# Kernel tuning notes

Measured on AMD Instinct MI355X. Metric: run time of the kernel, lower is better.

## Reference

```python
import jax, jax.numpy as jnp
import numpy as np

B, T, D, HS = 4, 4096, 512, 64


def setup_inputs() -> dict:
    key = jax.random.key(0)
    kx, kd, kk, kq, kv = jax.random.split(key, 5)
    X = jax.random.normal(kx, (B, T, D), dtype=jnp.float32)
    dag = jax.random.randint(kd, (T, T), 0, 2, dtype=jnp.int32)
    scale = 1.0 / np.sqrt(D).astype(np.float32)
    Wk = jax.random.normal(kk, (D, HS), dtype=jnp.float32) * scale
    Wq = jax.random.normal(kq, (D, HS), dtype=jnp.float32) * scale
    Wv = jax.random.normal(kv, (D, HS), dtype=jnp.float32) * scale
    return {"X": X, "dag": dag, "Wk": Wk, "Wq": Wq, "Wv": Wv}


def reference(X, dag, Wk, Wq, Wv):
    # Projections (nn.Linear without bias): [B,T,HS]
    K = X @ Wk
    Q = X @ Wq
    V = X @ Wv
    hs = Q.shape[-1]
    # Dense scores [B,T,T]
    QK = jnp.einsum('bid,bjd->bij', Q, K) / np.float32(np.sqrt(hs))
    mask = (dag == 0)  # [T,T], True -> -inf
    # Rows fully masked would softmax to NaN in torch; the module zeroes them.
    row_dead = jnp.all(mask, axis=-1)  # [T]
    neg_inf = jnp.asarray(-jnp.inf, QK.dtype)
    scores = jnp.where(mask, neg_inf, QK)
    # Neutralize dead rows before softmax to avoid NaN, then zero them out
    scores = jnp.where(row_dead[:, None], jnp.zeros((), QK.dtype), scores)
    att = jax.nn.softmax(scores, axis=-1)
    att = jnp.where(row_dead[:, None], jnp.zeros((), att.dtype), att)
    # Transposed AV matmul: out[b,j,h] = sum_i att[b,i,j] * V[b,i,h]
    out = jnp.einsum('bij,bih->bjh', att, V)
    # Swish activation
    return out * jax.nn.sigmoid(out)
```

## Files before the change

kernel.cpp:

```cpp
#include <hip/hip_runtime.h>
#include <hip/hip_bf16.h>
#include <math.h>

#define BB 4
#define TT 4096
#define DD 512
#define HH 64
#define TW 128

typedef unsigned int u32;
typedef unsigned short u16;
typedef float f32x16 __attribute__((ext_vector_type(16)));
typedef __bf16 bf16x8 __attribute__((ext_vector_type(8)));

#define SC 0.18033688011112042f

static __device__ __forceinline__ u16 f2b(float f) {
    __hip_bfloat16 h = __float2bfloat16(f);
    return __builtin_bit_cast(u16, h);
}
static __device__ __forceinline__ float b2f(u16 x) {
    return __builtin_bit_cast(float, (u32)x << 16);
}
static __device__ __forceinline__ u32 pk2(float a, float b) {
    return (u32)f2b(a) | ((u32)f2b(b) << 16);
}
static __device__ __forceinline__ bf16x8 ldf(const u16* p) {
    uint4 u = *(const uint4*)p;
    return __builtin_bit_cast(bf16x8, u);
}
static __device__ __forceinline__ bf16x8 c8(uint4 u) {
    return __builtin_bit_cast(bf16x8, u);
}
static __device__ __forceinline__ void swap32(u32& a, u32& b) {
    asm("v_permlane32_swap_b32 %0, %1" : "+v"(a), "+v"(b));
}


__global__ __launch_bounds__(256) void pack_kernel(const int* __restrict__ dag,
                                                   u32* __restrict__ bits2,
                                                   u32* __restrict__ bitsTT,
                                                   const float* __restrict__ Wq,
                                                   const float* __restrict__ Wk,
                                                   const float* __restrict__ Wv,
                                                   u16* __restrict__ Wt) {
    if (blockIdx.x >= 2048) {
        const int wb = blockIdx.x - 2048;
        const int m = wb >> 3, sub = wb & 7;
        const float* W = (m == 0) ? Wq : (m == 1) ? Wk : Wv;
        const int t = threadIdx.x;
        const int n = sub * 8 + (t >> 5);
        const int k0 = (t & 31) * 16;
        u16 buf[16];
#pragma unroll
        for (int k = 0; k < 16; ++k) buf[k] = f2b(W[(size_t)(k0 + k) * HH + n]);
        uint4* dst = (uint4*)(Wt + ((size_t)m * 64 + n) * DD + k0);
        dst[0] = *(uint4*)buf;
        dst[1] = *(uint4*)(buf + 8);
        return;
    }
    const int unit = blockIdx.x * 4 + (threadIdx.x >> 6);
    const int lane = threadIdx.x & 63;
    const int i64 = unit >> 7;
    const int j32 = unit & 127;
    const int i = i64 * 64 + lane;
    const int* p = dag + (size_t)i * TT + j32 * 32;
    u32 rw = 0;
#pragma unroll
    for (int c = 0; c < 32; c += 4) {
        int4 v = *(const int4*)(p + c);
        rw |= (v.x != 0 ? 1u : 0u) << c;
        rw |= (v.y != 0 ? 1u : 0u) << (c + 1);
        rw |= (v.z != 0 ? 1u : 0u) << (c + 2);
        rw |= (v.w != 0 ? 1u : 0u) << (c + 3);
    }
    bits2[(size_t)j32 * TT + i] = rw;
    u32 myw = 0;
#pragma unroll
    for (int c = 0; c < 32; ++c) {
        unsigned long long m = __ballot((rw >> c) & 1);
        u32 part = (lane < 32) ? (u32)m : (u32)(m >> 32);
        if ((lane & 31) == c) myw = part;
    }
    bitsTT[(size_t)(i64 * 2 + (lane >> 5)) * TT + j32 * 32 + (lane & 31)] = myw;
}

__global__ __launch_bounds__(384) void proj_kernel(const float* __restrict__ X,
                                                   const u16* __restrict__ Wt,
                                                   u16* __restrict__ QF,
                                                   u16* __restrict__ KF,
                                                   u16* __restrict__ VF) {
    const int w = threadIdx.x >> 6, lane = threadIdx.x & 63;
    const int m = w % 3, rg = w / 3;
    const int l31 = lane & 31, hf = lane >> 5;
    const int tile = blockIdx.x * 2 + rg;
    const int row0 = tile * 32;
    const float* xr = X + (size_t)(row0 + l31) * DD + hf * 8;
    const u16* wbase = Wt + (size_t)m * 64 * DD + hf * 8;

    f32x16 acc[2] = {};

    for (int kt = 0; kt < 32; ++kt) {
        float4 x0 = *(const float4*)(xr + kt * 16);
        float4 x1 = *(const float4*)(xr + kt * 16 + 4);
        uint4 aw;
        aw.x = pk2(x0.x, x0.y);
        aw.y = pk2(x0.z, x0.w);
        aw.z = pk2(x1.x, x1.y);
        aw.w = pk2(x1.z, x1.w);
        bf16x8 xa = __builtin_bit_cast(bf16x8, aw);
        const u16* wk = wbase + kt * 16;
#pragma unroll
        for (int nt = 0; nt < 2; ++nt) {
            bf16x8 wb = ldf(wk + (size_t)(nt * 32 + l31) * DD);
            acc[nt] = __builtin_amdgcn_mfma_f32_32x32x16_bf16(xa, wb, acc[nt], 0, 0, 0);
        }
    }
    const float sc = (m == 0) ? SC : 1.0f;
    if (m < 2) {
        u16* dst = (m == 0) ? QF : KF;
        const int kth = l31 >> 4, hfp = (l31 >> 3) & 1, e = l31 & 7;
#pragma unroll
        for (int nt = 0; nt < 2; ++nt)
#pragma unroll
            for (int r = 0; r < 16; ++r) {
                int rl = (r & 3) + 8 * (r >> 2) + 4 * hf;
                dst[(size_t)tile * 2048 + (nt * 2 + kth) * 512 + (rl + hfp * 32) * 8 + e]
                    = f2b(acc[nt][r] * sc);
            }
    } else {
#pragma unroll
        for (int nt = 0; nt < 2; ++nt)
#pragma unroll
            for (int r = 0; r < 16; ++r) {
                int rl = (r & 3) + 8 * (r >> 2) + 4 * hf;
                VF[(size_t)tile * 2048 + (nt * 2 + (rl >> 4)) * 512
                   + (l31 + ((rl >> 3) & 1) * 32) * 8 + (rl & 7)] = f2b(acc[nt][r]);
            }
    }
}

__global__ __launch_bounds__(512, 2) void stats_kernel(const u16* __restrict__ QF,
                                                       const u16* __restrict__ KF,
                                                       const u32* __restrict__ bits2,
                                                       float* __restrict__ cOut) {
    __shared__ float Lsh[8][128];
    const int bid = blockIdx.x;
    const int b = (bid & 7) >> 1;
    const int u = (bid & 1) * 32 + (bid >> 3);
    const int itg0 = u * 2;
    const int i0 = itg0 * 32;
    const int w = threadIdx.x >> 6, lane = threadIdx.x & 63;
    const int l31 = lane & 31, hf = lane >> 5;

    bf16x8 qfA[4], qfB[4];
    const u16* qbase = QF + (size_t)(b * 128 + itg0) * 2048 + lane * 8;
#pragma unroll
    for (int kt = 0; kt < 4; ++kt) {
        qfA[kt] = ldf(qbase + kt * 512);
        qfB[kt] = ldf(qbase + 2048 + kt * 512);
    }

    const u16* kf0 = KF + (size_t)b * 128 * 2048 + lane * 8;

    float LpA = 0.f, LpB = 0.f;
    for (int t = 0; t < 16; ++t) {
        const int jt = w + t * 8;
        const u16* kb = kf0 + (size_t)jt * 2048;
        u32 mwA = bits2[(size_t)jt * TT + i0 + l31];
        u32 mwB = bits2[(size_t)jt * TT + i0 + 32 + l31];

        bf16x8 k0 = ldf(kb), k1 = ldf(kb + 512), k2 = ldf(kb + 1024), k3 = ldf(kb + 1536);
        __builtin_amdgcn_s_setprio(1);
        f32x16 sA = {}, sB = {};
        sA = __builtin_amdgcn_mfma_f32_32x32x16_bf16(k0, qfA[0], sA, 0, 0, 0);
        sB = __builtin_amdgcn_mfma_f32_32x32x16_bf16(k0, qfB[0], sB, 0, 0, 0);
        sA = __builtin_amdgcn_mfma_f32_32x32x16_bf16(k1, qfA[1], sA, 0, 0, 0);
        sB = __builtin_amdgcn_mfma_f32_32x32x16_bf16(k1, qfB[1], sB, 0, 0, 0);
        sA = __builtin_amdgcn_mfma_f32_32x32x16_bf16(k2, qfA[2], sA, 0, 0, 0);
        sB = __builtin_amdgcn_mfma_f32_32x32x16_bf16(k2, qfB[2], sB, 0, 0, 0);
        sA = __builtin_amdgcn_mfma_f32_32x32x16_bf16(k3, qfA[3], sA, 0, 0, 0);
        sB = __builtin_amdgcn_mfma_f32_32x32x16_bf16(k3, qfB[3], sB, 0, 0, 0);
        __builtin_amdgcn_s_setprio(0);
        u32 mrA = __builtin_amdgcn_alignbit(mwA, mwA, hf * 4);
        u32 mrB = __builtin_amdgcn_alignbit(mwB, mwB, hf * 4);
#pragma unroll
        for (int r = 0; r < 16; ++r) {
            const int pos = (r & 3) + 8 * (r >> 2);
            float eA = __builtin_amdgcn_exp2f(sA[r]);
            float eB = __builtin_amdgcn_exp2f(sB[r]);
            LpA += ((mrA >> pos) & 1) ? eA : 0.f;
            LpB += ((mrB >> pos) & 1) ? eB : 0.f;
        }
    }
    Lsh[w][lane] = LpA;
    Lsh[w][64 + lane] = LpB;
    __syncthreads();
    if (threadIdx.x < 64) {
        const int g = threadIdx.x >> 5, il = threadIdx.x & 31;
        float L = 0.f;
#pragma unroll
        for (int q = 0; q < 8; ++q) L += Lsh[q][g * 64 + il] + Lsh[q][g * 64 + il + 32];
        cOut[(size_t)b * TT + i0 + g * 32 + il] = (L > 0.f) ? 1.f / L : 0.f;
    }
}

__global__ __launch_bounds__(256) void scalev_kernel(const u16* __restrict__ VF,
                                                     const float* __restrict__ cB,
                                                     u16* __restrict__ VF2) {
    const int bid = blockIdx.x;
    const int b = (bid & 7) >> 1;
    const int itg = (bid & 1) * 64 + (bid >> 3);
    const int tile = b * 128 + itg;
    const int q = threadIdx.x >> 6, ln = threadIdx.x & 63;
    const float* c = cB + (size_t)b * TT + itg * 32 + (q & 1) * 16 + (ln >> 5) * 8;
    float4 c0 = *(const float4*)c;
    float4 c1 = *(const float4*)(c + 4);
    const u16* p = VF + (size_t)tile * 2048 + q * 512 + ln * 8;
    uint4 v = *(const uint4*)p;
    u16* ve = (u16*)&v;
    ve[0] = f2b(b2f(ve[0]) * c0.x);
    ve[1] = f2b(b2f(ve[1]) * c0.y);
    ve[2] = f2b(b2f(ve[2]) * c0.z);
    ve[3] = f2b(b2f(ve[3]) * c0.w);
    ve[4] = f2b(b2f(ve[4]) * c1.x);
    ve[5] = f2b(b2f(ve[5]) * c1.y);
    ve[6] = f2b(b2f(ve[6]) * c1.z);
    ve[7] = f2b(b2f(ve[7]) * c1.w);
    *(uint4*)(VF2 + (size_t)tile * 2048 + q * 512 + ln * 8) = v;
}

__global__ __launch_bounds__(512, 2) void out_kernel(const u16* __restrict__ QF,
                                                     const u16* __restrict__ KF,
                                                     const u16* __restrict__ VF2,
                                                     const u32* __restrict__ bitsTT,
                                                     float* __restrict__ out) {
    __shared__ float red[2][4][2048];
    const int bid = blockIdx.x;
    const int b = (bid & 7) >> 1;
    const int u = (bid & 1) * 32 + (bid >> 3);
    const int jt0 = u * 2;
    const int j0 = jt0 * 32;
    const int w = threadIdx.x >> 6, lane = threadIdx.x & 63;
    const int l31 = lane & 31, hf = lane >> 5;

    bf16x8 kfA[4], kfB[4];
    const u16* kbase = KF + (size_t)(b * 128 + jt0) * 2048 + lane * 8;
#pragma unroll
    for (int kt = 0; kt < 4; ++kt) {
        kfA[kt] = ldf(kbase + kt * 512);
        kfB[kt] = ldf(kbase + 2048 + kt * 512);
    }

    const u16* qf0 = QF + (size_t)b * 128 * 2048 + lane * 8;
    const u16* vf0 = VF2 + (size_t)b * 128 * 2048 + lane * 8;

    f32x16 accA0 = {}, accA1 = {}, accB0 = {}, accB1 = {};

    for (int t = 0; t < 16; ++t) {
        const int it = w + t * 8;
        const u16* qb = qf0 + (size_t)it * 2048;
        const u16* vb = vf0 + (size_t)it * 2048;
        u32 mwA = bitsTT[(size_t)it * TT + j0 + l31];
        u32 mwB = bitsTT[(size_t)it * TT + j0 + 32 + l31];

        bf16x8 q0 = ldf(qb), q1 = ldf(qb + 512), q2 = ldf(qb + 1024), q3 = ldf(qb + 1536);
        __builtin_amdgcn_s_setprio(1);
        f32x16 sA = {}, sB = {};
        sA = __builtin_amdgcn_mfma_f32_32x32x16_bf16(q0, kfA[0], sA, 0, 0, 0);
        sB = __builtin_amdgcn_mfma_f32_32x32x16_bf16(q0, kfB[0], sB, 0, 0, 0);
        sA = __builtin_amdgcn_mfma_f32_32x32x16_bf16(q1, kfA[1], sA, 0, 0, 0);
        sB = __builtin_amdgcn_mfma_f32_32x32x16_bf16(q1, kfB[1], sB, 0, 0, 0);
        sA = __builtin_amdgcn_mfma_f32_32x32x16_bf16(q2, kfA[2], sA, 0, 0, 0);
        sB = __builtin_amdgcn_mfma_f32_32x32x16_bf16(q2, kfB[2], sB, 0, 0, 0);
        sA = __builtin_amdgcn_mfma_f32_32x32x16_bf16(q3, kfA[3], sA, 0, 0, 0);
        sB = __builtin_amdgcn_mfma_f32_32x32x16_bf16(q3, kfB[3], sB, 0, 0, 0);
        __builtin_amdgcn_s_setprio(0);

        u32 mrA = __builtin_amdgcn_alignbit(mwA, mwA, hf * 4);
        u32 mrB = __builtin_amdgcn_alignbit(mwB, mwB, hf * 4);

        float pA[16], pB[16];
#pragma unroll
        for (int r = 0; r < 16; ++r) {
            const int pos = (r & 3) + 8 * (r >> 2);
            float eA = __builtin_amdgcn_exp2f(sA[r]);
            float eB = __builtin_amdgcn_exp2f(sB[r]);
            pA[r] = ((mrA >> pos) & 1) ? eA : 0.f;
            pB[r] = ((mrB >> pos) & 1) ? eB : 0.f;
        }

        bf16x8 v00 = ldf(vb), v01 = ldf(vb + 512), v10 = ldf(vb + 1024), v11 = ldf(vb + 1536);

#pragma unroll
        for (int k2 = 0; k2 < 2; ++k2) {
            u32 aA  = pk2(pA[8 * k2 + 0], pA[8 * k2 + 1]);
            u32 bA  = pk2(pA[8 * k2 + 2], pA[8 * k2 + 3]);
            u32 cA  = pk2(pA[8 * k2 + 4], pA[8 * k2 + 5]);
            u32 dA  = pk2(pA[8 * k2 + 6], pA[8 * k2 + 7]);
            swap32(aA, cA);
            swap32(bA, dA);
            uint4 awA = {aA, bA, cA, dA};
            bf16x8 paA = __builtin_bit_cast(bf16x8, awA);
            u32 aB  = pk2(pB[8 * k2 + 0], pB[8 * k2 + 1]);
            u32 bB  = pk2(pB[8 * k2 + 2], pB[8 * k2 + 3]);
            u32 cB2 = pk2(pB[8 * k2 + 4], pB[8 * k2 + 5]);
            u32 dB  = pk2(pB[8 * k2 + 6], pB[8 * k2 + 7]);
            swap32(aB, cB2);
            swap32(bB, dB);
            uint4 awB = {aB, bB, cB2, dB};
            bf16x8 paB = __builtin_bit_cast(bf16x8, awB);
            bf16x8 v0 = (k2 == 0) ? v00 : v01;
            bf16x8 v1 = (k2 == 0) ? v10 : v11;
            __builtin_amdgcn_s_setprio(1);
            accA0 = __builtin_amdgcn_mfma_f32_32x32x16_bf16(paA, v0, accA0, 0, 0, 0);
            accB0 = __builtin_amdgcn_mfma_f32_32x32x16_bf16(paB, v0, accB0, 0, 0, 0);
            accA1 = __builtin_amdgcn_mfma_f32_32x32x16_bf16(paA, v1, accA1, 0, 0, 0);
            accB1 = __builtin_amdgcn_mfma_f32_32x32x16_bf16(paB, v1, accB1, 0, 0, 0);
            __builtin_amdgcn_s_setprio(0);
        }
    }

    if (w >= 4) {
#pragma unroll
        for (int r = 0; r < 16; ++r) {
            int jl = (r & 3) + 8 * (r >> 2) + 4 * hf;
            red[0][w - 4][jl * 64 + l31] = accA0[r];
            red[0][w - 4][jl * 64 + 32 + l31] = accA1[r];
            red[1][w - 4][jl * 64 + l31] = accB0[r];
            red[1][w - 4][jl * 64 + 32 + l31] = accB1[r];
        }
    }
    __syncthreads();
    if (w < 4) {
#pragma unroll
        for (int r = 0; r < 16; ++r) {
            int jl = (r & 3) + 8 * (r >> 2) + 4 * hf;
            red[0][w][jl * 64 + l31] += accA0[r];
            red[0][w][jl * 64 + 32 + l31] += accA1[r];
            red[1][w][jl * 64 + l31] += accB0[r];
            red[1][w][jl * 64 + 32 + l31] += accB1[r];
        }
    }
    __syncthreads();
    {
        const int idx = threadIdx.x * 8;
        const int g3 = idx >> 11, e = idx & 2047;
        float vv[8];
#pragma unroll
        for (int q = 0; q < 8; ++q) {
            int ee = e + q;
            float v = red[g3][0][ee] + red[g3][1][ee] + red[g3][2][ee] + red[g3][3][ee];
            vv[q] = v / (1.f + __expf(-v));
        }
        const int jl = e >> 6, hc = e & 63;
        float* dst = out + ((size_t)b * TT + (jt0 + g3) * 32 + jl) * HH + hc;
        *(float4*)dst = make_float4(vv[0], vv[1], vv[2], vv[3]);
        *(float4*)(dst + 4) = make_float4(vv[4], vv[5], vv[6], vv[7]);
    }
}

extern "C" void kernel_launch(void* const* d_in, const int* in_sizes, int n_in,
                              void* d_out, int out_size, void* d_ws, size_t ws_size,
                              hipStream_t stream) {
    const float* X  = (const float*)d_in[0];
    const int*  dag = (const int*)d_in[1];
    const float* Wk = (const float*)d_in[2];
    const float* Wq = (const float*)d_in[3];
    const float* Wv = (const float*)d_in[4];
    float* out = (float*)d_out;

    char* ws = (char*)d_ws;
    u16*   QF    = (u16*)ws;
    u16*   KF    = (u16*)(ws + (2u << 20));
    u16*   VF    = (u16*)(ws + (4u << 20));
    u16*   VF2   = (u16*)(ws + (6u << 20));
    u32*   bits2 = (u32*)(ws + (8u << 20));
    u32*   bitsTT= (u32*)(ws + (10u << 20));
    u16*   Wt    = (u16*)(ws + (12u << 20));
    float* cB    = (float*)(ws + (12u << 20) + (256u << 10));

    pack_kernel<<<2048 + 24, 256, 0, stream>>>(dag, bits2, bitsTT, Wq, Wk, Wv, Wt);
    proj_kernel<<<256, 384, 0, stream>>>(X, Wt, QF, KF, VF);
    stats_kernel<<<256, 512, 0, stream>>>(QF, KF, bits2, cB);
    scalev_kernel<<<512, 256, 0, stream>>>(VF, cB, VF2);
    out_kernel<<<256, 512, 0, stream>>>(QF, KF, VF2, bitsTT, out);
}
```

Baseline: 94.52 us.

## Fuse V scaling into stats kernel and co-schedule dag packing with projection

The separate V-scaling kernel is folded into the end of the stats kernel: each block keeps its row normalisers in shared memory and scales its own two V tiles, so the cB round trip through global memory and one launch go away. The dag bit-packing moves into the projection kernel as extra blocks, so packing and projection run in one launch and can overlap. Weight transposition becomes its own small kernel that runs ahead. The extra packing blocks are launched with 384 threads and 128 of them exit at once, which wastes some slots. The stats kernel also gains a tail phase with an extra barrier.

```diff
diff --git a/kernel.cpp b/kernel.cpp
--- a/kernel.cpp
+++ b/kernel.cpp
@@ -29,67 +29,65 @@
     uint4 u = *(const uint4*)p;
     return __builtin_bit_cast(bf16x8, u);
 }
-static __device__ __forceinline__ bf16x8 c8(uint4 u) {
-    return __builtin_bit_cast(bf16x8, u);
-}
 static __device__ __forceinline__ void swap32(u32& a, u32& b) {
     asm("v_permlane32_swap_b32 %0, %1" : "+v"(a), "+v"(b));
 }
 
 
-__global__ __launch_bounds__(256) void pack_kernel(const int* __restrict__ dag,
-                                                   u32* __restrict__ bits2,
-                                                   u32* __restrict__ bitsTT,
-                                                   const float* __restrict__ Wq,
-                                                   const float* __restrict__ Wk,
-                                                   const float* __restrict__ Wv,
-                                                   u16* __restrict__ Wt) {
-    if (blockIdx.x >= 2048) {
-        const int wb = blockIdx.x - 2048;
-        const int m = wb >> 3, sub = wb & 7;
-        const float* W = (m == 0) ? Wq : (m == 1) ? Wk : Wv;
-        const int t = threadIdx.x;
-        const int n = sub * 8 + (t >> 5);
-        const int k0 = (t & 31) * 16;
-        u16 buf[16];
-#pragma unroll
-        for (int k = 0; k < 16; ++k) buf[k] = f2b(W[(size_t)(k0 + k) * HH + n]);
-        uint4* dst = (uint4*)(Wt + ((size_t)m * 64 + n) * DD + k0);
-        dst[0] = *(uint4*)buf;
-        dst[1] = *(uint4*)(buf + 8);
+__global__ __launch_bounds__(256) void wtr_kernel(const float* __restrict__ Wq,
+                                                  const float* __restrict__ Wk,
+                                                  const float* __restrict__ Wv,
+                                                  u16* __restrict__ Wt) {
+    const int wb = blockIdx.x;
+    const int m = wb >> 3, sub = wb & 7;
+    const float* W = (m == 0) ? Wq : (m == 1) ? Wk : Wv;
+    const int t = threadIdx.x;
+    const int n = sub * 8 + (t >> 5);
+    const int k0 = (t & 31) * 16;
+    u16 buf[16];
+#pragma unroll
+    for (int k = 0; k < 16; ++k) buf[k] = f2b(W[(size_t)(k0 + k) * HH + n]);
+    uint4* dst = (uint4*)(Wt + ((size_t)m * 64 + n) * DD + k0);
+    dst[0] = *(uint4*)buf;
+    dst[1] = *(uint4*)(buf + 8);
+}
+
+__global__ __launch_bounds__(384) void pp_kernel(const float* __restrict__ X,
+                                                 const u16* __restrict__ Wt,
+                                                 u16* __restrict__ QF,
+                                                 u16* __restrict__ KF,
+                                                 u16* __restrict__ VF,
+                                                 const int* __restrict__ dag,
+                                                 u32* __restrict__ bits2,
+                                                 u32* __restrict__ bitsTT) {
+    if (blockIdx.x >= 256) {
+        if (threadIdx.x >= 256) return;
+        const int unit = (blockIdx.x - 256) * 4 + (threadIdx.x >> 6);
+        const int lane = threadIdx.x & 63;
+        const int i64 = unit >> 7;
+        const int j32 = unit & 127;
+        const int i = i64 * 64 + lane;
+        const int* p = dag + (size_t)i * TT + j32 * 32;
+        u32 rw = 0;
+#pragma unroll
+        for (int c = 0; c < 32; c += 4) {
+            int4 v = *(const int4*)(p + c);
+            rw |= (v.x != 0 ? 1u : 0u) << c;
+            rw |= (v.y != 0 ? 1u : 0u) << (c + 1);
+            rw |= (v.z != 0 ? 1u : 0u) << (c + 2);
+            rw |= (v.w != 0 ? 1u : 0u) << (c + 3);
+        }
+        bits2[(size_t)j32 * TT + i] = rw;
+        u32 myw = 0;
+#pragma unroll
+        for (int c = 0; c < 32; ++c) {
+            unsigned long long m = __ballot((rw >> c) & 1);
+            u32 part = (lane < 32) ? (u32)m : (u32)(m >> 32);
+            if ((lane & 31) == c) myw = part;
+        }
+        bitsTT[(size_t)(i64 * 2 + (lane >> 5)) * TT + j32 * 32 + (lane & 31)] = myw;
         return;
     }
-    const int unit = blockIdx.x * 4 + (threadIdx.x >> 6);
-    const int lane = threadIdx.x & 63;
-    const int i64 = unit >> 7;
-    const int j32 = unit & 127;
-    const int i = i64 * 64 + lane;
-    const int* p = dag + (size_t)i * TT + j32 * 32;
-    u32 rw = 0;
-#pragma unroll
-    for (int c = 0; c < 32; c += 4) {
-        int4 v = *(const int4*)(p + c);
-        rw |= (v.x != 0 ? 1u : 0u) << c;
-        rw |= (v.y != 0 ? 1u : 0u) << (c + 1);
-        rw |= (v.z != 0 ? 1u : 0u) << (c + 2);
-        rw |= (v.w != 0 ? 1u : 0u) << (c + 3);
-    }
-    bits2[(size_t)j32 * TT + i] = rw;
-    u32 myw = 0;
-#pragma unroll
-    for (int c = 0; c < 32; ++c) {
-        unsigned long long m = __ballot((rw >> c) & 1);
-        u32 part = (lane < 32) ? (u32)m : (u32)(m >> 32);
-        if ((lane & 31) == c) myw = part;
-    }
-    bitsTT[(size_t)(i64 * 2 + (lane >> 5)) * TT + j32 * 32 + (lane & 31)] = myw;
-}
-
-__global__ __launch_bounds__(384) void proj_kernel(const float* __restrict__ X,
-                                                   const u16* __restrict__ Wt,
-                                                   u16* __restrict__ QF,
-                                                   u16* __restrict__ KF,
-                                                   u16* __restrict__ VF) {
     const int w = threadIdx.x >> 6, lane = threadIdx.x & 63;
     const int m = w % 3, rg = w / 3;
     const int l31 = lane & 31, hf = lane >> 5;
@@ -143,8 +141,10 @@
 __global__ __launch_bounds__(512, 2) void stats_kernel(const u16* __restrict__ QF,
                                                        const u16* __restrict__ KF,
                                                        const u32* __restrict__ bits2,
-                                                       float* __restrict__ cOut) {
+                                                       const u16* __restrict__ VF,
+                                                       u16* __restrict__ VF2) {
     __shared__ float Lsh[8][128];
+    __shared__ float cSh[64];
     const int bid = blockIdx.x;
     const int b = (bid & 7) >> 1;
     const int u = (bid & 1) * 32 + (bid >> 3);
@@ -201,33 +201,29 @@
         float L = 0.f;
 #pragma unroll
         for (int q = 0; q < 8; ++q) L += Lsh[q][g * 64 + il] + Lsh[q][g * 64 + il + 32];
-        cOut[(size_t)b * TT + i0 + g * 32 + il] = (L > 0.f) ? 1.f / L : 0.f;
-    }
-}
-
-__global__ __launch_bounds__(256) void scalev_kernel(const u16* __restrict__ VF,
-                                                     const float* __restrict__ cB,
-                                                     u16* __restrict__ VF2) {
-    const int bid = blockIdx.x;
-    const int b = (bid & 7) >> 1;
-    const int itg = (bid & 1) * 64 + (bid >> 3);
-    const int tile = b * 128 + itg;
-    const int q = threadIdx.x >> 6, ln = threadIdx.x & 63;
-    const float* c = cB + (size_t)b * TT + itg * 32 + (q & 1) * 16 + (ln >> 5) * 8;
-    float4 c0 = *(const float4*)c;
-    float4 c1 = *(const float4*)(c + 4);
-    const u16* p = VF + (size_t)tile * 2048 + q * 512 + ln * 8;
-    uint4 v = *(const uint4*)p;
-    u16* ve = (u16*)&v;
-    ve[0] = f2b(b2f(ve[0]) * c0.x);
-    ve[1] = f2b(b2f(ve[1]) * c0.y);
-    ve[2] = f2b(b2f(ve[2]) * c0.z);
-    ve[3] = f2b(b2f(ve[3]) * c0.w);
-    ve[4] = f2b(b2f(ve[4]) * c1.x);
-    ve[5] = f2b(b2f(ve[5]) * c1.y);
-    ve[6] = f2b(b2f(ve[6]) * c1.z);
-    ve[7] = f2b(b2f(ve[7]) * c1.w);
-    *(uint4*)(VF2 + (size_t)tile * 2048 + q * 512 + ln * 8) = v;
+        cSh[g * 32 + il] = (L > 0.f) ? 1.f / L : 0.f;
+    }
+    __syncthreads();
+    {
+        const int tl = threadIdx.x >> 8;
+        const int rem = threadIdx.x & 255;
+        const int q = rem >> 6, ln = rem & 63;
+        const int ib = tl * 32 + (q & 1) * 16 + (ln >> 5) * 8;
+        float4 c0 = *(const float4*)&cSh[ib];
+        float4 c1 = *(const float4*)&cSh[ib + 4];
+        const size_t off = (size_t)(b * 128 + itg0 + tl) * 2048 + q * 512 + ln * 8;
+        uint4 v = *(const uint4*)(VF + off);
+        u16* ve = (u16*)&v;
+        ve[0] = f2b(b2f(ve[0]) * c0.x);
+        ve[1] = f2b(b2f(ve[1]) * c0.y);
+        ve[2] = f2b(b2f(ve[2]) * c0.z);
+        ve[3] = f2b(b2f(ve[3]) * c0.w);
+        ve[4] = f2b(b2f(ve[4]) * c1.x);
+        ve[5] = f2b(b2f(ve[5]) * c1.y);
+        ve[6] = f2b(b2f(ve[6]) * c1.z);
+        ve[7] = f2b(b2f(ve[7]) * c1.w);
+        *(uint4*)(VF2 + off) = v;
+    }
 }
 
 __global__ __launch_bounds__(512, 2) void out_kernel(const u16* __restrict__ QF,
@@ -378,11 +374,9 @@
     u32*   bits2 = (u32*)(ws + (8u << 20));
     u32*   bitsTT= (u32*)(ws + (10u << 20));
     u16*   Wt    = (u16*)(ws + (12u << 20));
-    float* cB    = (float*)(ws + (12u << 20) + (256u << 10));
-
-    pack_kernel<<<2048 + 24, 256, 0, stream>>>(dag, bits2, bitsTT, Wq, Wk, Wv, Wt);
-    proj_kernel<<<256, 384, 0, stream>>>(X, Wt, QF, KF, VF);
-    stats_kernel<<<256, 512, 0, stream>>>(QF, KF, bits2, cB);
-    scalev_kernel<<<512, 256, 0, stream>>>(VF, cB, VF2);
+
+    wtr_kernel<<<24, 256, 0, stream>>>(Wq, Wk, Wv, Wt);
+    pp_kernel<<<256 + 2048, 384, 0, stream>>>(X, Wt, QF, KF, VF, dag, bits2, bitsTT);
+    stats_kernel<<<256, 512, 0, stream>>>(QF, KF, bits2, VF, VF2);
     out_kernel<<<256, 512, 0, stream>>>(QF, KF, VF2, bitsTT, out);
 }
```

After: 91.19 us. 3.5% less time.
